# Performance work log

Measured on AMD Instinct MI355X. Metric: run time of the kernel, lower is better.

The kernel has to match this reference:

```python
import jax, jax.numpy as jnp
import numpy as np

DIM = 512
N = 64
DIV = 8
H = DIM // DIV  # 64
BATCH = 8
L_SEQ = 2048


def _kernel_dplr(Lam, P, B, C, step, L):
    # Lam: (N,) complex, P: (N,1), B: (N,H), C: (H,N), step: scalar
    omega = jnp.exp(-2j * jnp.pi * (jnp.arange(L) / L))        # (L,)
    g = (2.0 / step) * (1.0 - omega) / (1.0 + omega)           # (L,) generating-fn nodes
    c = 2.0 / (1.0 + omega)                                    # (L,)
    r = 1.0 / (g[:, None] - Lam[None, :])                      # (L,N) Cauchy resolvent
    Cc = jnp.conj(C)                                           # (H,N)
    p = P[:, 0]                                                # (N,)
    pc = jnp.conj(p)
    # vectorized Cauchy dot-products (torch version loops over L)
    k00 = jnp.einsum('in,nj,ln->lij', Cc, B, r)                # (L,H,H)
    k01 = jnp.einsum('in,n,ln->li', Cc, p, r)                  # (L,H)
    k10 = jnp.einsum('n,nj,ln->lj', pc, B, r)                  # (L,H)
    k11 = jnp.einsum('n,n,ln->l', pc, p, r)                    # (L,)
    # woodbury correction: inv(1 + k11) is a 1x1 batched inverse -> elementwise
    at_roots = c[:, None, None] * (
        k00 - k01[:, :, None] * (1.0 / (1.0 + k11))[:, None, None] * k10[:, None, :]
    )                                                          # (L,H,H)
    return jnp.fft.ifft(at_roots, n=L, axis=0).real            # (L,H,H)


def _fft_conv(u, K):
    # u: (b,L,H) real, K: (L,H,H) real. Linear conv via length-2L FFT.
    L = K.shape[0]
    ud = jnp.fft.rfft(u, n=2 * L, axis=1)                      # (b,Lf,H)
    Kd = jnp.fft.rfft(K, n=2 * L, axis=0)                      # (Lf,H,H)
    yf = jnp.einsum('lij,blj->bli', Kd, ud)                    # (b,Lf,H)
    return jnp.fft.irfft(yf, n=2 * L, axis=1)[:, :L]           # (b,L,H)


def reference(u, Lambda_re, Lambda_im, P_re, P_im, B_re, B_im, C_re, C_im, step):
    # straight-through clamp of Lambda_re (torch does an in-place no_grad clamp)
    Lambda_re = Lambda_re + jax.lax.stop_gradient(
        jnp.minimum(Lambda_re, -1e-4) - Lambda_re)
    Lam = Lambda_re + 1j * Lambda_im                           # (N,div)
    P = P_re + 1j * P_im                                       # (N,1,div)
    Bm = B_re + 1j * B_im                                      # (N,H,div)
    Cm = C_re + 1j * C_im                                      # (H,N,div)
    b, L, d = u.shape
    u4 = u.reshape(b, L, d // DIV, DIV)                        # (b,L,H,div)
    s = jnp.exp(step)[0]
    K = jax.vmap(_kernel_dplr, in_axes=(-1, -1, -1, -1, None, None),
                 out_axes=-1)(Lam, P, Bm, Cm, s, L)            # (L,H,H,div)
    y = jax.vmap(_fft_conv, in_axes=(-1, -1), out_axes=-1)(u4, K)  # (b,L,H,div)
    return y.reshape(b, L, d)


def setup_inputs() -> dict:
    key = jax.random.key(0)
    ks = jax.random.split(key, 10)
    sc = 0.5 ** 0.5
    u = jax.random.normal(ks[0], (BATCH, L_SEQ, DIM), dtype=jnp.float32)
    Lambda_re = -(jax.random.uniform(ks[1], (N, DIV), dtype=jnp.float32) * 0.5 + 0.1)
    Lambda_im = jax.random.normal(ks[2], (N, DIV), dtype=jnp.float32)
    P_re = jax.random.normal(ks[3], (N, 1, DIV), dtype=jnp.float32) * sc
    P_im = jax.random.normal(ks[4], (N, 1, DIV), dtype=jnp.float32) * sc
    B_re = jax.random.normal(ks[5], (N, H, DIV), dtype=jnp.float32) * sc
    B_im = jax.random.normal(ks[6], (N, H, DIV), dtype=jnp.float32) * sc
    C_re = jax.random.normal(ks[7], (H, N, DIV), dtype=jnp.float32) * sc
    C_im = jax.random.normal(ks[8], (H, N, DIV), dtype=jnp.float32) * sc
    step = jax.random.uniform(ks[9], (1,), dtype=jnp.float32,
                              minval=float(np.log(0.001)), maxval=float(np.log(0.1)))
    return {"u": u, "Lambda_re": Lambda_re, "Lambda_im": Lambda_im,
            "P_re": P_re, "P_im": P_im, "B_re": B_re, "B_im": B_im,
            "C_re": C_re, "C_im": C_im, "step": step}
```

## Files before the change

### kernel.cpp

```cpp
#include <hip/hip_runtime.h>
#include <hip/hip_bf16.h>
#include <math.h>

#define LSEQ 2048
#define NM   64
#define HD   64
#define NDIV 8
#define NB   8
#define NF   2049
#define NFP  2052
#define ATROWS 4224

#define SL(E) ((E) ^ (((E) >> 4) & 15))
#define FFT_BUF 2048

typedef __attribute__((ext_vector_type(8))) short bf16x8;
typedef __attribute__((ext_vector_type(4))) float f32x4;

__device__ __forceinline__ unsigned pack_c(float2 v) {
  __hip_bfloat162 h = __float22bfloat162_rn(v);
  return *reinterpret_cast<unsigned*>(&h);
}
__device__ __forceinline__ float2 unpack_c(unsigned u) {
  __hip_bfloat162 h = *reinterpret_cast<__hip_bfloat162*>(&u);
  return __bfloat1622float2(h);
}
__device__ __forceinline__ unsigned short f2bf(float v) {
  __hip_bfloat16 h = __float2bfloat16(v);
  return *reinterpret_cast<unsigned short*>(&h);
}

struct cplxd { double x, y; };
__device__ __forceinline__ cplxd cmuld(cplxd a, cplxd b) {
  return {a.x*b.x - a.y*b.y, a.x*b.y + a.y*b.x};
}
__device__ __forceinline__ cplxd cdivd(cplxd a, cplxd b) {
  double inv = 1.0 / (b.x*b.x + b.y*b.y);
  return {(a.x*b.x + a.y*b.y)*inv, (a.y*b.x - a.x*b.y)*inv};
}

template<int SIGN, int M>
__device__ __forceinline__ void r4_stage(const float2* __restrict__ src,
                                         float2* __restrict__ dst) {
  constexpr int L = 2048 / (4 * M);
  __syncthreads();
  #pragma unroll
  for (int t = 0; t < 2; t++) {
    int idx = (int)threadIdx.x + t * 256;
    int q = idx / M;
    int p = idx & (M - 1);
    float2 a0 = src[SL(idx)];
    float2 a1 = src[SL(idx + 512)];
    float2 a2 = src[SL(idx + 1024)];
    float2 a3 = src[SL(idx + 1536)];
    float2 b1, b2, b3;
    if constexpr (M > 1) {
      float s, c;
      __sincosf(-3.14159265358979324f * (float)(p * L) * (1.0f/1024.0f), &s, &c);
      float2 W1 = make_float2(c, (SIGN > 0) ? -s : s);
      float2 W2 = make_float2(W1.x*W1.x - W1.y*W1.y, 2.f*W1.x*W1.y);
      float2 W3 = make_float2(W2.x*W1.x - W2.y*W1.y, W2.x*W1.y + W2.y*W1.x);
      b1 = make_float2(a1.x*W1.x - a1.y*W1.y, a1.x*W1.y + a1.y*W1.x);
      b2 = make_float2(a2.x*W2.x - a2.y*W2.y, a2.x*W2.y + a2.y*W2.x);
      b3 = make_float2(a3.x*W3.x - a3.y*W3.y, a3.x*W3.y + a3.y*W3.x);
    } else { b1 = a1; b2 = a2; b3 = a3; }
    float2 e0 = make_float2(a0.x + b2.x, a0.y + b2.y);
    float2 e1 = make_float2(b1.x + b3.x, b1.y + b3.y);
    float2 d0 = make_float2(a0.x - b2.x, a0.y - b2.y);
    float2 d1 = make_float2(b1.x - b3.x, b1.y - b3.y);
    float2 o1, o3;
    if (SIGN < 0) { o1 = make_float2(d0.x + d1.y, d0.y - d1.x);
                    o3 = make_float2(d0.x - d1.y, d0.y + d1.x); }
    else          { o1 = make_float2(d0.x - d1.y, d0.y + d1.x);
                    o3 = make_float2(d0.x + d1.y, d0.y - d1.x); }
    int ob = q * 4 * M + p;
    dst[SL(ob)]         = make_float2(e0.x + e1.x, e0.y + e1.y);
    dst[SL(ob + M)]     = o1;
    dst[SL(ob + 2*M)]   = make_float2(e0.x - e1.x, e0.y - e1.y);
    dst[SL(ob + 3*M)]   = o3;
  }
}

template<int SIGN>
__device__ __forceinline__ void r4_mid(float2* a, float2* b) {
  r4_stage<SIGN,   4>(a, b);
  r4_stage<SIGN,  16>(b, a);
  r4_stage<SIGN,  64>(a, b);
  r4_stage<SIGN, 256>(b, a);
}

template<int SIGN>
__device__ __forceinline__ void r2f_ldst(const float2* __restrict__ src,
                                         float2* __restrict__ dst) {
  __syncthreads();
  #pragma unroll
  for (int t = 0; t < 4; t++) {
    int p = (int)threadIdx.x + t * 256;
    float2 a = src[SL(p)], b = src[SL(p + 1024)];
    float s, c;
    __sincosf(-6.28318530717958647f * (float)p * (1.0f/2048.0f), &s, &c);
    float wy = (SIGN > 0) ? -s : s;
    float2 wb = make_float2(b.x*c - b.y*wy, b.x*wy + b.y*c);
    dst[SL(p)]        = make_float2(a.x + wb.x, a.y + wb.y);
    dst[SL(p + 1024)] = make_float2(a.x - wb.x, a.y - wb.y);
  }
}

__device__ __forceinline__ void r4g_bf16_inv(const unsigned* __restrict__ row,
                                             float2* __restrict__ dst) {
  #pragma unroll
  for (int t = 0; t < 2; t++) {
    int idx = (int)threadIdx.x + t * 256;
    float2 a0 = unpack_c(row[idx]);
    float2 a1 = unpack_c(row[idx + 512]);
    float2 a2 = unpack_c(row[idx + 1024]);
    float2 a3 = unpack_c(row[idx + 1536]);
    float2 e0 = make_float2(a0.x + a2.x, a0.y + a2.y);
    float2 e1 = make_float2(a1.x + a3.x, a1.y + a3.y);
    float2 d0 = make_float2(a0.x - a2.x, a0.y - a2.y);
    float2 d1 = make_float2(a1.x - a3.x, a1.y - a3.y);
    float2 o1 = make_float2(d0.x - d1.y, d0.y + d1.x);
    float2 o3 = make_float2(d0.x + d1.y, d0.y - d1.x);
    int ob = idx * 4;
    dst[SL(ob)]   = make_float2(e0.x + e1.x, e0.y + e1.y);
    dst[SL(ob+1)] = o1;
    dst[SL(ob+2)] = make_float2(e0.x - e1.x, e0.y - e1.y);
    dst[SL(ob+3)] = o3;
  }
}

__device__ __forceinline__ void r4g_f32pad_fwd(const float2* __restrict__ g,
                                               float2* __restrict__ dst) {
  #pragma unroll
  for (int t = 0; t < 2; t++) {
    int idx = (int)threadIdx.x + t * 256;
    float2 a0 = g[idx];
    float2 a1 = g[idx + 512];
    int ob = idx * 4;
    dst[SL(ob)]   = make_float2(a0.x + a1.x, a0.y + a1.y);
    dst[SL(ob+1)] = make_float2(a0.x + a1.y, a0.y - a1.x);
    dst[SL(ob+2)] = make_float2(a0.x - a1.x, a0.y - a1.y);
    dst[SL(ob+3)] = make_float2(a0.x - a1.y, a0.y + a1.x);
  }
}

__device__ __forceinline__ void r4_modfused(const float2* __restrict__ pre,
                                            float2* __restrict__ dst) {
  __syncthreads();
  const float sc = 1.0f/2048.0f;
  const float R = 0.70710678118654752f;
  #pragma unroll
  for (int t = 0; t < 2; t++) {
    int idx = (int)threadIdx.x + t * 256;
    float a0x = pre[SL(idx)].x;
    float a1x = pre[SL(idx + 512)].x;
    float2 bA = pre[SL(idx + 1024)];
    float2 bB = pre[SL(idx + 1536)];
    float sA, cA, sB, cB;
    __sincosf(-6.28318530717958647f * (float)idx * (1.0f/2048.0f), &sA, &cA);
    __sincosf(-6.28318530717958647f * (float)(idx + 512) * (1.0f/2048.0f), &sB, &cB);
    float rA = bA.x*cA + bA.y*sA;
    float rB = bB.x*cB + bB.y*sB;
    float k0 = (a0x + rA) * sc;
    float k1 = (a1x + rB) * sc;
    float k2 = (a0x - rA) * sc;
    float k3 = (a1x - rB) * sc;
    float s, c;
    __sincosf(-3.14159265358979324f * (float)idx * (1.0f/2048.0f), &s, &c);
    float2 a0 = make_float2(k0*c,         k0*s);
    float2 a1 = make_float2(k1*R*(c + s), k1*R*(s - c));
    float2 a2 = make_float2(k2*s,        -k2*c);
    float2 a3 = make_float2(k3*R*(s - c), -k3*R*(s + c));
    float2 e0 = make_float2(a0.x + a2.x, a0.y + a2.y);
    float2 e1 = make_float2(a1.x + a3.x, a1.y + a3.y);
    float2 d0 = make_float2(a0.x - a2.x, a0.y - a2.y);
    float2 d1 = make_float2(a1.x - a3.x, a1.y - a3.y);
    float2 o1 = make_float2(d0.x + d1.y, d0.y - d1.x);
    float2 o3 = make_float2(d0.x - d1.y, d0.y + d1.x);
    int ob = idx * 4;
    dst[SL(ob)]   = make_float2(e0.x + e1.x, e0.y + e1.y);
    dst[SL(ob+1)] = o1;
    dst[SL(ob+2)] = make_float2(e0.x - e1.x, e0.y - e1.y);
    dst[SL(ob+3)] = o3;
  }
}

__device__ __forceinline__ void r2f_gw_bf16(const float2* __restrict__ src,
                                            unsigned* __restrict__ row) {
  __syncthreads();
  #pragma unroll
  for (int t = 0; t < 4; t++) {
    int p = (int)threadIdx.x + t * 256;
    float2 a = src[SL(p)], b = src[SL(p + 1024)];
    float s, c;
    __sincosf(-6.28318530717958647f * (float)p * (1.0f/2048.0f), &s, &c);
    float2 wb = make_float2(b.x*c - b.y*s, b.x*s + b.y*c);
    row[2*p + 1] = pack_c(make_float2(a.x + wb.x, a.y + wb.y));
  }
}

__device__ __forceinline__ void r2f_gw_f32h(const float2* __restrict__ src,
                                            float2* __restrict__ dst) {
  __syncthreads();
  const float sc = 1.0f/2048.0f;
  #pragma unroll
  for (int t = 0; t < 4; t++) {
    int p = (int)threadIdx.x + t * 256;
    float2 a = src[SL(p)], b = src[SL(p + 1024)];
    float s, c;
    __sincosf(-6.28318530717958647f * (float)p * (1.0f/2048.0f), &s, &c);
    float wy = -s;
    float2 wb = make_float2(b.x*c - b.y*wy, b.x*wy + b.y*c);
    dst[p] = make_float2((a.x + wb.x)*sc, (a.y + wb.y)*sc);
  }
}

__global__ __launch_bounds__(256) void ssm_kt(
    const float* __restrict__ Cre, const float* __restrict__ Cim,
    const float* __restrict__ Bre, const float* __restrict__ Bim,
    const float* __restrict__ Pre, const float* __restrict__ Pim,
    float2* __restrict__ CT, float2* __restrict__ BT, float2* __restrict__ PT) {
  int idx = blockIdx.x * 256 + threadIdx.x;
  int dv = idx >> 12, n = (idx >> 6) & 63, x = idx & 63;
  CT[idx] = make_float2(Cre[((size_t)x*NM + n)*NDIV + dv], -Cim[((size_t)x*NM + n)*NDIV + dv]);
  BT[idx] = make_float2(Bre[((size_t)n*HD + x)*NDIV + dv],  Bim[((size_t)n*HD + x)*NDIV + dv]);
  if (idx < NDIV*NM) {
    int dv2 = idx >> 6, n2 = idx & 63;
    PT[idx] = make_float2(Pre[n2*NDIV + dv2], Pim[n2*NDIV + dv2]);
  }
}

__global__ __launch_bounds__(256) void ssm_k0a(
    const float* __restrict__ Lre, const float* __restrict__ Lim,
    const float* __restrict__ Pre, const float* __restrict__ Pim,
    const float* __restrict__ step, unsigned short* __restrict__ RBr,
    unsigned short* __restrict__ RBi, float2* __restrict__ cpx) {
  int idx = blockIdx.x * 256 + threadIdx.x;
  int qn = idx & 3;
  int rest = idx >> 2;
  int l = rest & (LSEQ - 1);
  int dv = rest >> 11;
  double s = (double)expf(step[0]);
  float angf = -6.2831855f * ((float)l * (1.0f/2048.0f));
  double si, co;
  sincos((double)angf, &si, &co);
  cplxd om    = {co, si};
  cplxd one_p = {1.0 + om.x,  om.y};
  double ts = 2.0 / s;
  cplxd g = cdivd({ts*(1.0 - om.x), ts*(-om.y)}, one_p);
  cplxd c = cdivd({2.0, 0.0}, one_p);
  double k11x = 0.0, k11y = 0.0;
  for (int u = 0; u < 16; u++) {
    int n = qn*16 + u;
    float lre = fminf(Lre[n*NDIV+dv], -0.0001f);
    float lim = Lim[n*NDIV+dv];
    cplxd den = {g.x - (double)lre, g.y - (double)lim};
    cplxd r   = cdivd({1.0, 0.0}, den);
    cplxd rcv = cmuld(c, r);
    size_t bidx = (((size_t)(dv*8 + (n >> 3)))*LSEQ + l)*8 + (n & 7);
    RBr[bidx] = f2bf((float)rcv.x);
    RBi[bidx] = f2bf((float)rcv.y);
    double pr = (double)Pre[n*NDIV+dv], pi = (double)Pim[n*NDIV+dv];
    double p2 = pr*pr + pi*pi;
    k11x += p2 * rcv.x; k11y += p2 * rcv.y;
  }
  k11x += __shfl_xor(k11x, 1); k11y += __shfl_xor(k11y, 1);
  k11x += __shfl_xor(k11x, 2); k11y += __shfl_xor(k11y, 2);
  if (qn == 0)
    cpx[(size_t)dv*LSEQ + l] = make_float2((float)(c.x + k11x), (float)(c.y + k11y));
}

__global__ __launch_bounds__(256) void ssm_km(
    const float2* __restrict__ CT, const float2* __restrict__ BT,
    const float2* __restrict__ PT, unsigned short* __restrict__ ATr,
    unsigned short* __restrict__ ATi, unsigned short* __restrict__ ATin) {
  __shared__ float2 PAN[4096];
  __shared__ float2 ROW[64];
  int dv = blockIdx.y;
  int ib = blockIdx.x;
  int tid = threadIdx.x;
  if (ib < 64) {
    for (int q = tid; q < 4096; q += 256) PAN[q] = BT[(size_t)dv*4096 + q];
    if (tid < 64) ROW[tid] = CT[(size_t)dv*4096 + tid*64 + ib];
    __syncthreads();
    int j = tid >> 2, nq = tid & 3;
    size_t rbase = ((size_t)dv*ATROWS + ib*64 + j)*64;
    for (int u = 0; u < 16; u++) {
      int n = nq*16 + u;
      float2 cv = ROW[n];
      float2 bv = PAN[n*64 + j];
      float xr = cv.x*bv.x - cv.y*bv.y, xi = cv.x*bv.y + cv.y*bv.x;
      ATr[rbase + n] = f2bf(xr); ATi[rbase + n] = f2bf(xi); ATin[rbase + n] = f2bf(-xi);
    }
  } else {
    for (int q = tid; q < 4096; q += 256) PAN[q] = CT[(size_t)dv*4096 + q];
    if (tid < 64) ROW[tid] = PT[dv*64 + tid];
    __syncthreads();
    int x = tid >> 2, nq = tid & 3;
    size_t pbase = ((size_t)dv*ATROWS + 4096 + x)*64;
    for (int u = 0; u < 16; u++) {
      int n = nq*16 + u;
      float2 cv = PAN[n*64 + x];
      float2 pv = ROW[n];
      float xr = cv.x*pv.x - cv.y*pv.y, xi = cv.x*pv.y + cv.y*pv.x;
      ATr[pbase + n] = f2bf(xr); ATi[pbase + n] = f2bf(xi); ATin[pbase + n] = f2bf(-xi);
    }
    __syncthreads();
    for (int q = tid; q < 4096; q += 256) PAN[q] = BT[(size_t)dv*4096 + q];
    __syncthreads();
    size_t qbase = ((size_t)dv*ATROWS + 4160 + x)*64;
    for (int u = 0; u < 16; u++) {
      int n = nq*16 + u;
      float2 bv = PAN[n*64 + x];
      float2 pv = ROW[n];
      float xr = pv.x*bv.x + pv.y*bv.y, xi = pv.x*bv.y - pv.y*bv.x;
      ATr[qbase + n] = f2bf(xr); ATi[qbase + n] = f2bf(xi); ATin[qbase + n] = f2bf(-xi);
    }
  }
}

__device__ __forceinline__ void gemm_core(
    const unsigned short* __restrict__ ATr, const unsigned short* __restrict__ ATi,
    const unsigned short* __restrict__ ATin, const unsigned short* __restrict__ RBr,
    const unsigned short* __restrict__ RBi, int dv, int mrow0, int l0, int lane,
    f32x4 accR[4], f32x4 accI[4]) {
  int mloc = lane & 15, kgrp = lane >> 4;
  #pragma unroll
  for (int t = 0; t < 4; t++) {
    accR[t] = (f32x4){0.f, 0.f, 0.f, 0.f};
    accI[t] = (f32x4){0.f, 0.f, 0.f, 0.f};
  }
  size_t abase = ((size_t)dv*ATROWS + mrow0 + mloc)*64 + kgrp*8;
  #pragma unroll
  for (int s = 0; s < 2; s++) {
    bf16x8 ar = *reinterpret_cast<const bf16x8*>(ATr  + abase + s*32);
    bf16x8 ai = *reinterpret_cast<const bf16x8*>(ATi  + abase + s*32);
    bf16x8 an = *reinterpret_cast<const bf16x8*>(ATin + abase + s*32);
    size_t bbase = (((size_t)(dv*8 + s*4 + kgrp))*LSEQ + l0 + mloc)*8;
    #pragma unroll
    for (int t = 0; t < 4; t++) {
      bf16x8 br = *reinterpret_cast<const bf16x8*>(RBr + bbase + t*128);
      bf16x8 bi = *reinterpret_cast<const bf16x8*>(RBi + bbase + t*128);
      accR[t] = __builtin_amdgcn_mfma_f32_16x16x32_bf16(ar, br, accR[t], 0, 0, 0);
      accR[t] = __builtin_amdgcn_mfma_f32_16x16x32_bf16(an, bi, accR[t], 0, 0, 0);
      accI[t] = __builtin_amdgcn_mfma_f32_16x16x32_bf16(ar, bi, accI[t], 0, 0, 0);
      accI[t] = __builtin_amdgcn_mfma_f32_16x16x32_bf16(ai, br, accI[t], 0, 0, 0);
    }
  }
}

__global__ __launch_bounds__(256) void ssm_g1(
    const unsigned short* __restrict__ ATr, const unsigned short* __restrict__ ATi,
    const unsigned short* __restrict__ ATin, const unsigned short* __restrict__ RBr,
    const unsigned short* __restrict__ RBi, const float2* __restrict__ cpx,
    float2* __restrict__ A1h, float2* __restrict__ K10h) {
  int which = blockIdx.x;
  int nBlk = blockIdx.y;
  int dv = blockIdx.z;
  int wave = threadIdx.x >> 6, lane = threadIdx.x & 63;
  int mrow0 = 4096 + which*64 + wave*16;
  int l0 = nBlk * 64;
  f32x4 accR[4], accI[4];
  gemm_core(ATr, ATi, ATin, RBr, RBi, dv, mrow0, l0, lane, accR, accI);
  int rbase = (lane >> 4) * 4;
  #pragma unroll
  for (int t = 0; t < 4; t++) {
    int l = l0 + t*16 + (lane & 15);
    if (which == 0) {
      float2 w = cpx[((size_t)dv << 11) + l];
      float inv = 1.0f / (w.x*w.x + w.y*w.y);
      #pragma unroll
      for (int r = 0; r < 4; r++) {
        int x = wave*16 + rbase + r;
        float sx = accR[t][r], sy = accI[t][r];
        A1h[((size_t)(dv*64 + x))*LSEQ + l] =
            make_float2((sx*w.x + sy*w.y)*inv, (sy*w.x - sx*w.y)*inv);
      }
    } else {
      #pragma unroll
      for (int r = 0; r < 4; r++) {
        int x = wave*16 + rbase + r;
        K10h[((size_t)(dv*LSEQ + l))*64 + x] = make_float2(accR[t][r], accI[t][r]);
      }
    }
  }
}

__global__ __launch_bounds__(256) void ssm_g2(
    const unsigned short* __restrict__ ATr, const unsigned short* __restrict__ ATi,
    const unsigned short* __restrict__ ATin, const unsigned short* __restrict__ RBr,
    const unsigned short* __restrict__ RBi, const float2* __restrict__ A1h,
    const float2* __restrict__ K10h, unsigned* __restrict__ big, int dv) {
  int mBlk = blockIdx.x;
  int nBlk = blockIdx.y;
  int wave = threadIdx.x >> 6, lane = threadIdx.x & 63;
  int mrow0 = mBlk*64 + wave*16;
  int l0 = nBlk * 64;
  f32x4 accR[4], accI[4];
  gemm_core(ATr, ATi, ATin, RBr, RBi, dv, mrow0, l0, lane, accR, accI);
  int rbase = (lane >> 4) * 4;
  #pragma unroll
  for (int t = 0; t < 4; t++) {
    int l = l0 + t*16 + (lane & 15);
    float2 a1 = A1h[((size_t)(dv*64 + mBlk))*LSEQ + l];
    const float2* kp = K10h + ((size_t)(dv*LSEQ + l))*64 + wave*16 + rbase;
    #pragma unroll
    for (int r = 0; r < 4; r++) {
      float2 k10 = kp[r];
      float cx = a1.x*k10.x - a1.y*k10.y;
      float cy = a1.x*k10.y + a1.y*k10.x;
      int chain = mBlk*64 + wave*16 + rbase + r;
      big[(size_t)chain*NFP + l] = pack_c(make_float2(accR[t][r] - cx, accI[t][r] - cy));
    }
  }
}

__global__ __launch_bounds__(256) void ssm_ku(const float* __restrict__ u, float* __restrict__ ut) {
  __shared__ float s[16][513];
  int b  = blockIdx.x >> 7;
  int l0 = (blockIdx.x & 127) << 4;
  int tid = threadIdx.x;
  for (int q = tid; q < 16*512; q += 256) {
    int ll = q >> 9, dd = q & 511;
    s[ll][dd] = u[((size_t)b*LSEQ + l0 + ll)*512 + dd];
  }
  __syncthreads();
  for (int q = tid; q < 16*512; q += 256) {
    int d = q >> 4, ll = q & 15;
    int dvv = d & 7, h = d >> 3;
    ut[(((size_t)(dvv*NB + b))*HD + h)*LSEQ + l0 + ll] = s[ll][d];
  }
}

__global__ __launch_bounds__(256) void ssm_k3(const float* __restrict__ ut,
                                              unsigned* __restrict__ ud, int cbase) {
  __shared__ float2 b0[FFT_BUF];
  __shared__ float2 b1[FFT_BUF];
  int tid = threadIdx.x;
  const float2* src = (const float2*)(ut + ((size_t)(cbase + blockIdx.x)) * LSEQ);
  unsigned* dst = ud + (size_t)blockIdx.x * NF;
  r4g_f32pad_fwd(src, b1);
  r4_mid<-1>(b1, b0);
  r2f_ldst<-1>(b1, b0);
  __syncthreads();
  for (int f = tid; f <= 2048; f += 256) {
    int fa = f & 2047, fb = (2048 - f) & 2047;
    float2 Zf = b0[SL(fa)];
    float2 Zm = b0[SL(fb)];
    float Ex = (Zf.x + Zm.x)*0.5f, Ey = (Zf.y - Zm.y)*0.5f;
    float Dx = Zf.x - Zm.x,        Dy = Zf.y + Zm.y;
    float Ox = Dy*0.5f, Oy = -Dx*0.5f;
    float s, c2;
    __sincosf(-6.28318530717958647f * (float)f * (1.0f/4096.0f), &s, &c2);
    float WOx = Ox*c2 - Oy*s, WOy = Ox*s + Oy*c2;
    dst[f] = pack_c(make_float2(Ex + WOx, Ey + WOy));
  }
}

__global__ __launch_bounds__(256) void ssm_k2(unsigned* __restrict__ big) {
  __shared__ float2 b0[FFT_BUF];
  __shared__ float2 b1[FFT_BUF];
  int tid = threadIdx.x;
  unsigned* row = big + (size_t)blockIdx.x * NFP;
  float2 ev[4];
  #pragma unroll
  for (int k = 0; k < 4; k++) {
    int l = tid + 256*k;
    float2 a = unpack_c(row[l]);
    float2 b = unpack_c(row[(2048 - l) & 2047]);
    ev[k] = make_float2((a.x + b.x)*0.5f, (a.y - b.y)*0.5f);
  }
  float ev1024 = (tid == 0) ? unpack_c(row[1024]).x : 0.f;
  r4g_bf16_inv(row, b1);
  __syncthreads();
  #pragma unroll
  for (int k = 0; k < 4; k++) { int l = tid + 256*k; row[2*l] = pack_c(ev[k]); }
  if (tid == 0) row[2048] = pack_c(make_float2(ev1024, 0.f));
  r4_mid<1>(b1, b0);
  r4_modfused(b1, b0);
  r4_mid<-1>(b0, b1);
  r2f_gw_bf16(b0, row);
}

__global__ __launch_bounds__(256) void ssm_k4(
    const unsigned* __restrict__ kdt, const unsigned* __restrict__ ud,
    float2* __restrict__ yf) {
  __shared__ unsigned uds[NB][64][8];
  int tid = threadIdx.x;
  int f0 = blockIdx.x * 8;
  int i0 = blockIdx.y * 16;
  int ii = tid >> 4;
  int jj = (tid >> 2) & 3;
  int fl = tid & 3;
  int i = i0 + ii;
  for (int q = tid; q < NB*64*8; q += 256) {
    int b = q >> 9, j = (q >> 3) & 63, fq = q & 7;
    int f_ = f0 + fq;
    uds[b][j][fq] = (f_ < NF) ? ud[((size_t)(b*HD + j))*NF + f_] : 0u;
  }
  __syncthreads();
  float2 acc[2][NB];
  #pragma unroll
  for (int e = 0; e < 2; e++)
    #pragma unroll
    for (int b = 0; b < NB; b++) acc[e][b] = make_float2(0.f, 0.f);
  #pragma unroll 4
  for (int jt = 0; jt < 16; jt++) {
    int j = jj*16 + jt;
    const unsigned* kp = kdt + ((size_t)(i*HD + j))*NFP + f0 + fl*2;
    uint2 kq = *reinterpret_cast<const uint2*>(kp);
    float2 kv0 = unpack_c(kq.x);
    float2 kv1 = unpack_c(kq.y);
    #pragma unroll
    for (int b = 0; b < NB; b++) {
      float2 u0 = unpack_c(uds[b][j][fl*2]);
      float2 u1 = unpack_c(uds[b][j][fl*2 + 1]);
      acc[0][b].x += kv0.x*u0.x - kv0.y*u0.y;
      acc[0][b].y += kv0.x*u0.y + kv0.y*u0.x;
      acc[1][b].x += kv1.x*u1.x - kv1.y*u1.y;
      acc[1][b].y += kv1.x*u1.y + kv1.y*u1.x;
    }
  }
  #pragma unroll
  for (int e = 0; e < 2; e++)
    #pragma unroll
    for (int b = 0; b < NB; b++) {
      acc[e][b].x += __shfl_xor(acc[e][b].x, 4);
      acc[e][b].y += __shfl_xor(acc[e][b].y, 4);
      acc[e][b].x += __shfl_xor(acc[e][b].x, 8);
      acc[e][b].y += __shfl_xor(acc[e][b].y, 8);
    }
  if (jj == 0) {
    #pragma unroll
    for (int b = 0; b < NB; b++) {
      size_t base = ((size_t)(b*HD + i))*NF + f0 + fl*2;
      #pragma unroll
      for (int e = 0; e < 2; e++)
        if (f0 + fl*2 + e < NF) yf[base + e] = acc[e][b];
    }
  }
}

__global__ __launch_bounds__(256) void ssm_k5(const float2* __restrict__ yf,
                                              float* __restrict__ yt, int dv) {
  __shared__ float2 b0[FFT_BUF];
  __shared__ float2 b1[FFT_BUF];
  int tid = threadIdx.x;
  int b = blockIdx.x >> 6, i = blockIdx.x & 63;
  const float2* src = yf + (size_t)(b*HD + i) * NF;
  float2* dst = (float2*)(yt + (((size_t)(dv*NB + b))*HD + i) * LSEQ);
  for (int k = tid; k < 2048; k += 256) {
    float2 Xk = src[k];
    float2 Xm = src[2048 - k];
    float Ex = (Xk.x + Xm.x)*0.5f, Ey = (Xk.y - Xm.y)*0.5f;
    float Dx = Xk.x - Xm.x,        Dy = Xk.y + Xm.y;
    float s, c;
    __sincosf(6.28318530717958647f * (float)k * (1.0f/4096.0f), &s, &c);
    float Ox = 0.5f*(Dx*c - Dy*s);
    float Oy = 0.5f*(Dx*s + Dy*c);
    b0[SL(k)] = make_float2(Ex - Oy, Ey + Ox);
  }
  r4_stage<1, 1>(b0, b1);
  r4_mid<1>(b1, b0);
  r2f_gw_f32h(b1, dst);
}

__global__ __launch_bounds__(256) void ssm_t2(const float* __restrict__ yt, float* __restrict__ out) {
  __shared__ float s[512][17];
  int b  = blockIdx.x >> 7;
  int t0 = (blockIdx.x & 127) << 4;
  int tid = threadIdx.x;
  for (int q = tid; q < 512*16; q += 256) {
    int d = q >> 4, tt = q & 15;
    int dvv = d & 7, i = d >> 3;
    s[d][tt] = yt[(((size_t)(dvv*NB + b))*HD + i)*LSEQ + t0 + tt];
  }
  __syncthreads();
  for (int q = tid; q < 512*16; q += 256) {
    int tt = q >> 9, d = q & 511;
    out[((size_t)b*LSEQ + t0 + tt)*512 + d] = s[d][tt];
  }
}

extern "C" void kernel_launch(void* const* d_in, const int* in_sizes, int n_in,
                              void* d_out, int out_size, void* d_ws, size_t ws_size,
                              hipStream_t stream) {
  const float* u    = (const float*)d_in[0];
  const float* Lre  = (const float*)d_in[1];
  const float* Lim  = (const float*)d_in[2];
  const float* Pre  = (const float*)d_in[3];
  const float* Pim  = (const float*)d_in[4];
  const float* Bre  = (const float*)d_in[5];
  const float* Bim  = (const float*)d_in[6];
  const float* Cre  = (const float*)d_in[7];
  const float* Cim  = (const float*)d_in[8];
  const float* step = (const float*)d_in[9];
  float* out = (float*)d_out;

  char* w = (char*)d_ws;
  size_t off = 0;
  auto carve = [&](size_t bytes) -> void* {
    void* p = (void*)(w + off);
    off += (bytes + 255) & ~(size_t)255;
    return p;
  };
  float2*   cpx  = (float2*)carve((size_t)NDIV*LSEQ*sizeof(float2));
  float*    ut   = (float*) carve((size_t)NDIV*NB*HD*LSEQ*sizeof(float));
  unsigned* big  = (unsigned*)carve((size_t)4096*NFP*sizeof(unsigned) + 256);
  float2*   yf   = (float2*)carve((size_t)512*NF*sizeof(float2));
  float2*   CT   = (float2*)carve((size_t)NDIV*NM*HD*sizeof(float2));
  float2*   BT   = (float2*)carve((size_t)NDIV*NM*HD*sizeof(float2));
  float2*   PT   = (float2*)carve((size_t)NDIV*NM*sizeof(float2));
  unsigned short* ATr  = (unsigned short*)carve((size_t)NDIV*ATROWS*64*2);
  unsigned short* ATi  = (unsigned short*)carve((size_t)NDIV*ATROWS*64*2);
  unsigned short* ATin = (unsigned short*)carve((size_t)NDIV*ATROWS*64*2);
  unsigned short* RBr  = (unsigned short*)carve((size_t)NDIV*8*LSEQ*8*2);
  unsigned short* RBi  = (unsigned short*)carve((size_t)NDIV*8*LSEQ*8*2);
  float2*   A1h  = (float2*)carve((size_t)NDIV*64*LSEQ*sizeof(float2));
  float2*   K10h = (float2*)carve((size_t)NDIV*LSEQ*64*sizeof(float2));
  size_t off_m = off;
  unsigned* ud_full = (unsigned*)carve((size_t)NDIV*512*NF*sizeof(unsigned));
  bool full = (ws_size >= off);
  unsigned* ud = ud_full;
  if (!full) {
    off = off_m;
    ud = (unsigned*)carve((size_t)512*NF*sizeof(unsigned));
    if (ws_size < off) return;
  }
  (void)in_sizes; (void)n_in; (void)out_size;

  ssm_kt<<<128, 256, 0, stream>>>(Cre, Cim, Bre, Bim, Pre, Pim, CT, BT, PT);
  ssm_k0a<<<256, 256, 0, stream>>>(Lre, Lim, Pre, Pim, step, RBr, RBi, cpx);
  ssm_km<<<dim3(65, 8), 256, 0, stream>>>(CT, BT, PT, ATr, ATi, ATin);
  ssm_ku<<<1024, 256, 0, stream>>>(u, ut);
  ssm_g1<<<dim3(2, 32, 8), 256, 0, stream>>>(ATr, ATi, ATin, RBr, RBi, cpx, A1h, K10h);
  if (full) ssm_k3<<<4096, 256, 0, stream>>>(ut, ud_full, 0);
  for (int dv = 0; dv < NDIV; ++dv) {
    if (!full) ssm_k3<<<512, 256, 0, stream>>>(ut, ud, dv*512);
    const unsigned* udp = full ? (ud_full + (size_t)dv*512*NF) : ud;
    ssm_g2<<<dim3(64, 32), 256, 0, stream>>>(ATr, ATi, ATin, RBr, RBi, A1h, K10h, big, dv);
    ssm_k2<<<4096, 256, 0, stream>>>(big);
    ssm_k4<<<dim3(257, 4), 256, 0, stream>>>(big, udp, yf);
    ssm_k5<<<512, 256, 0, stream>>>(yf, ut, dv);
  }
  ssm_t2<<<1024, 256, 0, stream>>>(ut, out);
}
```

Measured before the change: 896.6 us.

## Replace radix-4/2 shared-memory FFT stages with radix-8 stages

Rewrites the 2048-point in-block FFTs used in the forward input transform, kernel generation and inverse output transform from six radix-4/radix-2 passes to three radix-8 passes plus one radix-4 pass. This cuts the number of shared-memory round trips and __syncthreads barriers per FFT, and reduces twiddle evaluations. In exchange each thread holds 8 complex values, which raises register pressure, and the modulation and last-stage fusions are restructured, which could introduce index or sign errors.

Result: faster. 867.2 us, median of 2 (-3.3%).

```diff
diff --git a/kernel.cpp b/kernel.cpp
--- a/kernel.cpp
+++ b/kernel.cpp
@@ -30,6 +30,12 @@
   return *reinterpret_cast<unsigned short*>(&h);
 }
 
+__device__ __forceinline__ float2 cadd(float2 a, float2 b) { return make_float2(a.x+b.x, a.y+b.y); }
+__device__ __forceinline__ float2 csub(float2 a, float2 b) { return make_float2(a.x-b.x, a.y-b.y); }
+__device__ __forceinline__ float2 cmulf(float2 a, float2 b) {
+  return make_float2(a.x*b.x - a.y*b.y, a.x*b.y + a.y*b.x);
+}
+
 struct cplxd { double x, y; };
 __device__ __forceinline__ cplxd cmuld(cplxd a, cplxd b) {
   return {a.x*b.x - a.y*b.y, a.x*b.y + a.y*b.x};
@@ -39,179 +45,202 @@
   return {(a.x*b.x + a.y*b.y)*inv, (a.y*b.x - a.x*b.y)*inv};
 }
 
+template<int SIGN>
+__device__ __forceinline__ void dft8(float2* a) {
+  const float R = 0.70710678118654752f;
+  float2 e0 = cadd(a[0], a[4]), e1 = cadd(a[2], a[6]);
+  float2 d0 = csub(a[0], a[4]), d1 = csub(a[2], a[6]);
+  float2 t0 = cadd(e0, e1), t2 = csub(e0, e1);
+  float2 t1, t3;
+  if (SIGN < 0) { t1 = make_float2(d0.x + d1.y, d0.y - d1.x);
+                  t3 = make_float2(d0.x - d1.y, d0.y + d1.x); }
+  else          { t1 = make_float2(d0.x - d1.y, d0.y + d1.x);
+                  t3 = make_float2(d0.x + d1.y, d0.y - d1.x); }
+  float2 f0 = cadd(a[1], a[5]), f1 = cadd(a[3], a[7]);
+  float2 g0 = csub(a[1], a[5]), g1 = csub(a[3], a[7]);
+  float2 s0 = cadd(f0, f1), s2 = csub(f0, f1);
+  float2 s1, s3;
+  if (SIGN < 0) { s1 = make_float2(g0.x + g1.y, g0.y - g1.x);
+                  s3 = make_float2(g0.x - g1.y, g0.y + g1.x); }
+  else          { s1 = make_float2(g0.x - g1.y, g0.y + g1.x);
+                  s3 = make_float2(g0.x + g1.y, g0.y - g1.x); }
+  float2 r1, r2, r3;
+  if (SIGN < 0) {
+    r1 = make_float2(R*(s1.x + s1.y), R*(s1.y - s1.x));
+    r2 = make_float2(s2.y, -s2.x);
+    r3 = make_float2(R*(s3.y - s3.x), -R*(s3.x + s3.y));
+  } else {
+    r1 = make_float2(R*(s1.x - s1.y), R*(s1.x + s1.y));
+    r2 = make_float2(-s2.y, s2.x);
+    r3 = make_float2(-R*(s3.x + s3.y), R*(s3.x - s3.y));
+  }
+  a[0] = cadd(t0, s0); a[4] = csub(t0, s0);
+  a[1] = cadd(t1, r1); a[5] = csub(t1, r1);
+  a[2] = cadd(t2, r2); a[6] = csub(t2, r2);
+  a[3] = cadd(t3, r3); a[7] = csub(t3, r3);
+}
+
 template<int SIGN, int M>
-__device__ __forceinline__ void r4_stage(const float2* __restrict__ src,
+__device__ __forceinline__ void r8_stage(const float2* __restrict__ src,
                                          float2* __restrict__ dst) {
-  constexpr int L = 2048 / (4 * M);
+  __syncthreads();
+  int idx = (int)threadIdx.x;
+  int q = idx / M, p = idx - q*M;
+  float2 a[8];
+  #pragma unroll
+  for (int v = 0; v < 8; v++) a[v] = src[SL(idx + 256*v)];
+  if constexpr (M > 1) {
+    float s, c;
+    __sincosf(-6.28318530717958647f * (float)p / (8.0f * (float)M), &s, &c);
+    if (SIGN > 0) s = -s;
+    float2 W1 = make_float2(c, s);
+    float2 W2 = cmulf(W1, W1);
+    float2 W3 = cmulf(W2, W1);
+    float2 W4 = cmulf(W2, W2);
+    float2 W5 = cmulf(W3, W2);
+    float2 W6 = cmulf(W3, W3);
+    float2 W7 = cmulf(W4, W3);
+    a[1] = cmulf(a[1], W1); a[2] = cmulf(a[2], W2); a[3] = cmulf(a[3], W3);
+    a[4] = cmulf(a[4], W4); a[5] = cmulf(a[5], W5); a[6] = cmulf(a[6], W6);
+    a[7] = cmulf(a[7], W7);
+  }
+  dft8<SIGN>(a);
+  int ob = q * 8 * M + p;
+  #pragma unroll
+  for (int u = 0; u < 8; u++) dst[SL(ob + u*M)] = a[u];
+}
+
+__device__ __forceinline__ void r8g_bf16_inv(const unsigned* __restrict__ row,
+                                             float2* __restrict__ dst) {
+  int idx = (int)threadIdx.x;
+  float2 a[8];
+  #pragma unroll
+  for (int v = 0; v < 8; v++) a[v] = unpack_c(row[idx + 256*v]);
+  dft8<1>(a);
+  int ob = idx * 8;
+  #pragma unroll
+  for (int u = 0; u < 8; u++) dst[SL(ob + u)] = a[u];
+}
+
+__device__ __forceinline__ void r8g_f32pad_fwd(const float2* __restrict__ g,
+                                               float2* __restrict__ dst) {
+  int idx = (int)threadIdx.x;
+  float2 a[8];
+  #pragma unroll
+  for (int v = 0; v < 4; v++) a[v] = g[idx + 256*v];
+  #pragma unroll
+  for (int v = 4; v < 8; v++) a[v] = make_float2(0.f, 0.f);
+  dft8<-1>(a);
+  int ob = idx * 8;
+  #pragma unroll
+  for (int u = 0; u < 8; u++) dst[SL(ob + u)] = a[u];
+}
+
+template<int SIGN>
+__device__ __forceinline__ void r4f_ldst(const float2* __restrict__ src,
+                                         float2* __restrict__ dst) {
   __syncthreads();
   #pragma unroll
   for (int t = 0; t < 2; t++) {
-    int idx = (int)threadIdx.x + t * 256;
-    int q = idx / M;
-    int p = idx & (M - 1);
-    float2 a0 = src[SL(idx)];
-    float2 a1 = src[SL(idx + 512)];
-    float2 a2 = src[SL(idx + 1024)];
-    float2 a3 = src[SL(idx + 1536)];
-    float2 b1, b2, b3;
-    if constexpr (M > 1) {
-      float s, c;
-      __sincosf(-3.14159265358979324f * (float)(p * L) * (1.0f/1024.0f), &s, &c);
-      float2 W1 = make_float2(c, (SIGN > 0) ? -s : s);
-      float2 W2 = make_float2(W1.x*W1.x - W1.y*W1.y, 2.f*W1.x*W1.y);
-      float2 W3 = make_float2(W2.x*W1.x - W2.y*W1.y, W2.x*W1.y + W2.y*W1.x);
-      b1 = make_float2(a1.x*W1.x - a1.y*W1.y, a1.x*W1.y + a1.y*W1.x);
-      b2 = make_float2(a2.x*W2.x - a2.y*W2.y, a2.x*W2.y + a2.y*W2.x);
-      b3 = make_float2(a3.x*W3.x - a3.y*W3.y, a3.x*W3.y + a3.y*W3.x);
-    } else { b1 = a1; b2 = a2; b3 = a3; }
-    float2 e0 = make_float2(a0.x + b2.x, a0.y + b2.y);
-    float2 e1 = make_float2(b1.x + b3.x, b1.y + b3.y);
-    float2 d0 = make_float2(a0.x - b2.x, a0.y - b2.y);
-    float2 d1 = make_float2(b1.x - b3.x, b1.y - b3.y);
+    int p = (int)threadIdx.x + t * 256;
+    float2 a0 = src[SL(p)], a1 = src[SL(p + 512)];
+    float2 a2 = src[SL(p + 1024)], a3 = src[SL(p + 1536)];
+    float s, c;
+    __sincosf(-6.28318530717958647f * (float)p * (1.0f/2048.0f), &s, &c);
+    if (SIGN > 0) s = -s;
+    float2 W1 = make_float2(c, s);
+    float2 W2 = cmulf(W1, W1);
+    float2 W3 = cmulf(W2, W1);
+    float2 b1 = cmulf(a1, W1), b2 = cmulf(a2, W2), b3 = cmulf(a3, W3);
+    float2 e0 = cadd(a0, b2), e1 = cadd(b1, b3);
+    float2 d0 = csub(a0, b2), d1 = csub(b1, b3);
     float2 o1, o3;
     if (SIGN < 0) { o1 = make_float2(d0.x + d1.y, d0.y - d1.x);
                     o3 = make_float2(d0.x - d1.y, d0.y + d1.x); }
     else          { o1 = make_float2(d0.x - d1.y, d0.y + d1.x);
                     o3 = make_float2(d0.x + d1.y, d0.y - d1.x); }
-    int ob = q * 4 * M + p;
-    dst[SL(ob)]         = make_float2(e0.x + e1.x, e0.y + e1.y);
-    dst[SL(ob + M)]     = o1;
-    dst[SL(ob + 2*M)]   = make_float2(e0.x - e1.x, e0.y - e1.y);
-    dst[SL(ob + 3*M)]   = o3;
-  }
-}
-
-template<int SIGN>
-__device__ __forceinline__ void r4_mid(float2* a, float2* b) {
-  r4_stage<SIGN,   4>(a, b);
-  r4_stage<SIGN,  16>(b, a);
-  r4_stage<SIGN,  64>(a, b);
-  r4_stage<SIGN, 256>(b, a);
-}
-
-template<int SIGN>
-__device__ __forceinline__ void r2f_ldst(const float2* __restrict__ src,
-                                         float2* __restrict__ dst) {
-  __syncthreads();
-  #pragma unroll
-  for (int t = 0; t < 4; t++) {
+    dst[SL(p)]        = cadd(e0, e1);
+    dst[SL(p + 512)]  = o1;
+    dst[SL(p + 1024)] = csub(e0, e1);
+    dst[SL(p + 1536)] = o3;
+  }
+}
+
+__device__ __forceinline__ void r4f_mod(const float2* __restrict__ src,
+                                        float2* __restrict__ dst) {
+  __syncthreads();
+  const float sc = 1.0f/2048.0f;
+  const float R = 0.70710678118654752f;
+  #pragma unroll
+  for (int t = 0; t < 2; t++) {
     int p = (int)threadIdx.x + t * 256;
-    float2 a = src[SL(p)], b = src[SL(p + 1024)];
+    float2 a0 = src[SL(p)], a1 = src[SL(p + 512)];
+    float2 a2 = src[SL(p + 1024)], a3 = src[SL(p + 1536)];
     float s, c;
     __sincosf(-6.28318530717958647f * (float)p * (1.0f/2048.0f), &s, &c);
-    float wy = (SIGN > 0) ? -s : s;
-    float2 wb = make_float2(b.x*c - b.y*wy, b.x*wy + b.y*c);
-    dst[SL(p)]        = make_float2(a.x + wb.x, a.y + wb.y);
-    dst[SL(p + 1024)] = make_float2(a.x - wb.x, a.y - wb.y);
-  }
-}
-
-__device__ __forceinline__ void r4g_bf16_inv(const unsigned* __restrict__ row,
-                                             float2* __restrict__ dst) {
+    float2 W1 = make_float2(c, -s);
+    float2 W2 = cmulf(W1, W1);
+    float2 W3 = cmulf(W2, W1);
+    float2 b1 = cmulf(a1, W1), b2 = cmulf(a2, W2), b3 = cmulf(a3, W3);
+    float2 e0 = cadd(a0, b2), e1 = cadd(b1, b3);
+    float2 d0 = csub(a0, b2), d1 = csub(b1, b3);
+    float kr0 = (e0.x + e1.x) * sc;
+    float kr1 = (d0.x - d1.y) * sc;
+    float kr2 = (e0.x - e1.x) * sc;
+    float kr3 = (d0.x + d1.y) * sc;
+    float ms, mc;
+    __sincosf(-3.14159265358979324f * (float)p * (1.0f/2048.0f), &ms, &mc);
+    dst[SL(p)]        = make_float2(kr0*mc,           kr0*ms);
+    dst[SL(p + 512)]  = make_float2(kr1*R*(mc + ms),  kr1*R*(ms - mc));
+    dst[SL(p + 1024)] = make_float2(kr2*ms,          -kr2*mc);
+    dst[SL(p + 1536)] = make_float2(kr3*R*(ms - mc), -kr3*R*(mc + ms));
+  }
+}
+
+__device__ __forceinline__ void r4f_gw_bf16(const float2* __restrict__ src,
+                                            unsigned* __restrict__ row) {
+  __syncthreads();
   #pragma unroll
   for (int t = 0; t < 2; t++) {
-    int idx = (int)threadIdx.x + t * 256;
-    float2 a0 = unpack_c(row[idx]);
-    float2 a1 = unpack_c(row[idx + 512]);
-    float2 a2 = unpack_c(row[idx + 1024]);
-    float2 a3 = unpack_c(row[idx + 1536]);
-    float2 e0 = make_float2(a0.x + a2.x, a0.y + a2.y);
-    float2 e1 = make_float2(a1.x + a3.x, a1.y + a3.y);
-    float2 d0 = make_float2(a0.x - a2.x, a0.y - a2.y);
-    float2 d1 = make_float2(a1.x - a3.x, a1.y - a3.y);
-    float2 o1 = make_float2(d0.x - d1.y, d0.y + d1.x);
-    float2 o3 = make_float2(d0.x + d1.y, d0.y - d1.x);
-    int ob = idx * 4;
-    dst[SL(ob)]   = make_float2(e0.x + e1.x, e0.y + e1.y);
-    dst[SL(ob+1)] = o1;
-    dst[SL(ob+2)] = make_float2(e0.x - e1.x, e0.y - e1.y);
-    dst[SL(ob+3)] = o3;
-  }
-}
-
-__device__ __forceinline__ void r4g_f32pad_fwd(const float2* __restrict__ g,
-                                               float2* __restrict__ dst) {
-  #pragma unroll
-  for (int t = 0; t < 2; t++) {
-    int idx = (int)threadIdx.x + t * 256;
-    float2 a0 = g[idx];
-    float2 a1 = g[idx + 512];
-    int ob = idx * 4;
-    dst[SL(ob)]   = make_float2(a0.x + a1.x, a0.y + a1.y);
-    dst[SL(ob+1)] = make_float2(a0.x + a1.y, a0.y - a1.x);
-    dst[SL(ob+2)] = make_float2(a0.x - a1.x, a0.y - a1.y);
-    dst[SL(ob+3)] = make_float2(a0.x - a1.y, a0.y + a1.x);
-  }
-}
-
-__device__ __forceinline__ void r4_modfused(const float2* __restrict__ pre,
-                                            float2* __restrict__ dst) {
-  __syncthreads();
-  const float sc = 1.0f/2048.0f;
-  const float R = 0.70710678118654752f;
-  #pragma unroll
-  for (int t = 0; t < 2; t++) {
-    int idx = (int)threadIdx.x + t * 256;
-    float a0x = pre[SL(idx)].x;
-    float a1x = pre[SL(idx + 512)].x;
-    float2 bA = pre[SL(idx + 1024)];
-    float2 bB = pre[SL(idx + 1536)];
-    float sA, cA, sB, cB;
-    __sincosf(-6.28318530717958647f * (float)idx * (1.0f/2048.0f), &sA, &cA);
-    __sincosf(-6.28318530717958647f * (float)(idx + 512) * (1.0f/2048.0f), &sB, &cB);
-    float rA = bA.x*cA + bA.y*sA;
-    float rB = bB.x*cB + bB.y*sB;
-    float k0 = (a0x + rA) * sc;
-    float k1 = (a1x + rB) * sc;
-    float k2 = (a0x - rA) * sc;
-    float k3 = (a1x - rB) * sc;
-    float s, c;
-    __sincosf(-3.14159265358979324f * (float)idx * (1.0f/2048.0f), &s, &c);
-    float2 a0 = make_float2(k0*c,         k0*s);
-    float2 a1 = make_float2(k1*R*(c + s), k1*R*(s - c));
-    float2 a2 = make_float2(k2*s,        -k2*c);
-    float2 a3 = make_float2(k3*R*(s - c), -k3*R*(s + c));
-    float2 e0 = make_float2(a0.x + a2.x, a0.y + a2.y);
-    float2 e1 = make_float2(a1.x + a3.x, a1.y + a3.y);
-    float2 d0 = make_float2(a0.x - a2.x, a0.y - a2.y);
-    float2 d1 = make_float2(a1.x - a3.x, a1.y - a3.y);
-    float2 o1 = make_float2(d0.x + d1.y, d0.y - d1.x);
-    float2 o3 = make_float2(d0.x - d1.y, d0.y + d1.x);
-    int ob = idx * 4;
-    dst[SL(ob)]   = make_float2(e0.x + e1.x, e0.y + e1.y);
-    dst[SL(ob+1)] = o1;
-    dst[SL(ob+2)] = make_float2(e0.x - e1.x, e0.y - e1.y);
-    dst[SL(ob+3)] = o3;
-  }
-}
-
-__device__ __forceinline__ void r2f_gw_bf16(const float2* __restrict__ src,
-                                            unsigned* __restrict__ row) {
-  __syncthreads();
-  #pragma unroll
-  for (int t = 0; t < 4; t++) {
     int p = (int)threadIdx.x + t * 256;
-    float2 a = src[SL(p)], b = src[SL(p + 1024)];
+    float2 a0 = src[SL(p)], a1 = src[SL(p + 512)];
+    float2 a2 = src[SL(p + 1024)], a3 = src[SL(p + 1536)];
     float s, c;
     __sincosf(-6.28318530717958647f * (float)p * (1.0f/2048.0f), &s, &c);
-    float2 wb = make_float2(b.x*c - b.y*s, b.x*s + b.y*c);
-    row[2*p + 1] = pack_c(make_float2(a.x + wb.x, a.y + wb.y));
-  }
-}
-
-__device__ __forceinline__ void r2f_gw_f32h(const float2* __restrict__ src,
+    float2 W1 = make_float2(c, s);
+    float2 W2 = cmulf(W1, W1);
+    float2 W3 = cmulf(W2, W1);
+    float2 b1 = cmulf(a1, W1), b2 = cmulf(a2, W2), b3 = cmulf(a3, W3);
+    float2 e0 = cadd(a0, b2), e1 = cadd(b1, b3);
+    float2 d0 = csub(a0, b2), d1 = csub(b1, b3);
+    float2 z0 = cadd(e0, e1);
+    float2 z1 = make_float2(d0.x + d1.y, d0.y - d1.x);
+    row[2*p + 1]       = pack_c(z0);
+    row[2*(p+512) + 1] = pack_c(z1);
+  }
+}
+
+__device__ __forceinline__ void r4f_gw_f32h(const float2* __restrict__ src,
                                             float2* __restrict__ dst) {
   __syncthreads();
   const float sc = 1.0f/2048.0f;
   #pragma unroll
-  for (int t = 0; t < 4; t++) {
+  for (int t = 0; t < 2; t++) {
     int p = (int)threadIdx.x + t * 256;
-    float2 a = src[SL(p)], b = src[SL(p + 1024)];
+    float2 a0 = src[SL(p)], a1 = src[SL(p + 512)];
+    float2 a2 = src[SL(p + 1024)], a3 = src[SL(p + 1536)];
     float s, c;
     __sincosf(-6.28318530717958647f * (float)p * (1.0f/2048.0f), &s, &c);
-    float wy = -s;
-    float2 wb = make_float2(b.x*c - b.y*wy, b.x*wy + b.y*c);
-    dst[p] = make_float2((a.x + wb.x)*sc, (a.y + wb.y)*sc);
+    float2 W1 = make_float2(c, -s);
+    float2 W2 = cmulf(W1, W1);
+    float2 W3 = cmulf(W2, W1);
+    float2 b1 = cmulf(a1, W1), b2 = cmulf(a2, W2), b3 = cmulf(a3, W3);
+    float2 e0 = cadd(a0, b2), e1 = cadd(b1, b3);
+    float2 d0 = csub(a0, b2), d1 = csub(b1, b3);
+    float2 z0 = cadd(e0, e1);
+    float2 z1 = make_float2(d0.x - d1.y, d0.y + d1.x);
+    dst[p]       = make_float2(z0.x*sc, z0.y*sc);
+    dst[p + 512] = make_float2(z1.x*sc, z1.y*sc);
   }
 }
 
@@ -439,9 +468,10 @@
   int tid = threadIdx.x;
   const float2* src = (const float2*)(ut + ((size_t)(cbase + blockIdx.x)) * LSEQ);
   unsigned* dst = ud + (size_t)blockIdx.x * NF;
-  r4g_f32pad_fwd(src, b1);
-  r4_mid<-1>(b1, b0);
-  r2f_ldst<-1>(b1, b0);
+  r8g_f32pad_fwd(src, b1);
+  r8_stage<-1, 8>(b1, b0);
+  r8_stage<-1, 64>(b0, b1);
+  r4f_ldst<-1>(b1, b0);
   __syncthreads();
   for (int f = tid; f <= 2048; f += 256) {
     int fa = f & 2047, fb = (2048 - f) & 2047;
@@ -471,15 +501,18 @@
     ev[k] = make_float2((a.x + b.x)*0.5f, (a.y - b.y)*0.5f);
   }
   float ev1024 = (tid == 0) ? unpack_c(row[1024]).x : 0.f;
-  r4g_bf16_inv(row, b1);
+  r8g_bf16_inv(row, b1);
   __syncthreads();
   #pragma unroll
   for (int k = 0; k < 4; k++) { int l = tid + 256*k; row[2*l] = pack_c(ev[k]); }
   if (tid == 0) row[2048] = pack_c(make_float2(ev1024, 0.f));
-  r4_mid<1>(b1, b0);
-  r4_modfused(b1, b0);
-  r4_mid<-1>(b0, b1);
-  r2f_gw_bf16(b0, row);
+  r8_stage<1, 8>(b1, b0);
+  r8_stage<1, 64>(b0, b1);
+  r4f_mod(b1, b0);
+  r8_stage<-1, 1>(b0, b1);
+  r8_stage<-1, 8>(b1, b0);
+  r8_stage<-1, 64>(b0, b1);
+  r4f_gw_bf16(b1, row);
 }
 
 __global__ __launch_bounds__(256) void ssm_k4(
@@ -560,9 +593,10 @@
     float Oy = 0.5f*(Dx*s + Dy*c);
     b0[SL(k)] = make_float2(Ex - Oy, Ey + Ox);
   }
-  r4_stage<1, 1>(b0, b1);
-  r4_mid<1>(b1, b0);
-  r2f_gw_f32h(b1, dst);
+  r8_stage<1, 1>(b0, b1);
+  r8_stage<1, 8>(b1, b0);
+  r8_stage<1, 64>(b0, b1);
+  r4f_gw_f32h(b1, dst);
 }
 
 __global__ __launch_bounds__(256) void ssm_t2(const float* __restrict__ yt, float* __restrict__ out) {
```
